# Kernel optimization log

Measured on AMD Instinct MI355X. Metric: run time of the kernel, lower is better.

## Reference

```python
import jax, jax.numpy as jnp
import numpy as np

N = 8192
F_IN = 256
F_OUT = 64
ALPHA = 0.2  # LeakyReLU negative slope
MASK_VAL = -9e15


def setup_inputs() -> dict:
    key = jax.random.key(0)
    k1, k2, k3, k4 = jax.random.split(key, 4)
    h = jax.random.normal(k1, (N, F_IN), dtype=jnp.float32)
    adj = jax.random.randint(k2, (N, N), 0, 2, dtype=jnp.int32)  # 0/1 dense adjacency
    # Parameters (original creates them inside forward with xavier init; here fixed inputs)
    W = jax.random.normal(k3, (F_IN, F_OUT), dtype=jnp.float32) * (1.414 * np.sqrt(2.0 / (F_IN + F_OUT)))
    a = jax.random.normal(k4, (2 * F_OUT, 1), dtype=jnp.float32) * (1.414 * np.sqrt(2.0 / (2 * F_OUT + 1)))
    return {"h": h, "adj": adj, "W": W, "a": a}


def reference(h, adj, W, a):
    # Wh: [N, F_OUT]
    Wh = h @ W
    # e_ij = LeakyReLU(a^T [Wh_i ; Wh_j]) computed via broadcast instead of the
    f_src = Wh @ a[:F_OUT, 0]   # [N] contribution of row node i
    f_dst = Wh @ a[F_OUT:, 0]   # [N] contribution of col node j
    e = jax.nn.leaky_relu(f_src[:, None] + f_dst[None, :], negative_slope=ALPHA)  # [N, N]
    # adj-masked row softmax
    scores = jnp.where(adj > 0, e, MASK_VAL)
    attention = jax.nn.softmax(scores, axis=1)
    # dropout omitted (deterministic eval reference)
    h_prime = attention @ Wh  # [N, F_OUT]
    return jax.nn.elu(h_prime)  # concat=True branch
```

## Files before the change

kernel.cpp:

```cpp
#include <hip/hip_runtime.h>
#include <hip/hip_bf16.h>

#define NN 8192
#define FIN 256
#define FOUT 64
#define L2E 1.4426950408889634f
#define PADK 40

typedef __attribute__((ext_vector_type(8))) short short8;
typedef __attribute__((ext_vector_type(4))) float f32x4;
typedef __attribute__((ext_vector_type(4))) int   iv4;

#define BAR() do { \
  __asm__ __volatile__("s_waitcnt lgkmcnt(0)" ::: "memory"); \
  __builtin_amdgcn_s_barrier(); \
  __asm__ __volatile__("" ::: "memory"); \
} while (0)

__device__ __forceinline__ unsigned short f2bf(float x){
  unsigned u = __float_as_uint(x);
  u += 0x7FFFu + ((u >> 16) & 1u);
  return (unsigned short)(u >> 16);
}

__global__ __launch_bounds__(256) void k_prep(const float* __restrict__ h,
    const float* __restrict__ W, const float* __restrict__ a,
    unsigned short* __restrict__ WhT, float* __restrict__ fs,
    float* __restrict__ fd, unsigned* __restrict__ gmax_u){
  __shared__ float Ws[128*64];
  __shared__ float hs[8][128];
  const int t = threadIdx.x, l = t & 63, wv = t >> 6;
  const int rb = blockIdx.x * 8;
  float acc0 = 0.f, acc1 = 0.f;
  for (int half = 0; half < 2; ++half){
    if (half) __syncthreads();
    for (int i = t; i < 2048; i += 256)
      ((float4*)Ws)[i] = ((const float4*)W)[half*2048 + i];
    {
      int rr = t >> 5, cc = t & 31;
      ((float4*)&hs[rr][0])[cc] =
          *(const float4*)(h + (size_t)(rb+rr)*FIN + half*128 + cc*4);
    }
    __syncthreads();
    #pragma unroll 8
    for (int k = 0; k < 128; ++k){
      float wval = Ws[k*64 + l];
      acc0 = fmaf(hs[wv*2+0][k], wval, acc0);
      acc1 = fmaf(hs[wv*2+1][k], wval, acc1);
    }
  }
  const int r0 = rb + wv*2, r1 = r0 + 1;
  float a1 = a[l], a2 = a[64 + l];
  float p0 = acc0*a1, q0 = acc0*a2, p1 = acc1*a1, q1 = acc1*a2;
  #pragma unroll
  for (int m = 1; m < 64; m <<= 1){
    p0 += __shfl_xor(p0, m); q0 += __shfl_xor(q0, m);
    p1 += __shfl_xor(p1, m); q1 += __shfl_xor(q1, m);
  }
  if (l == 0){
    fs[r0] = p0*L2E; fs[r1] = p1*L2E; fd[r0] = q0*L2E; fd[r1] = q1*L2E;
    atomicMax(gmax_u, __float_as_uint(q0*L2E + 64.0f));
    atomicMax(gmax_u, __float_as_uint(q1*L2E + 64.0f));
  }
  WhT[(size_t)l*NN + r0] = f2bf(acc0);
  WhT[(size_t)l*NN + r1] = f2bf(acc1);
}

struct ABuf { iv4 a0, a1; };

__device__ __forceinline__ void load_adj(ABuf& b, const int* __restrict__ adj,
                                         unsigned a_off, int s){
  const iv4* p = (const iv4*)(adj + a_off + s*32);
  b.a0 = __builtin_nontemporal_load(p);
  b.a1 = __builtin_nontemporal_load(p + 1);
}

__device__ __forceinline__ void attn_math(const ABuf& ab, f32x4 fv0, f32x4 fv1,
    short8 w0, short8 w1, short8 w2, short8 w3,
    float fsrL, float mL, f32x4* acc, float& s0, float& s1){
  const int   av[8] = {ab.a0.x,ab.a0.y,ab.a0.z,ab.a0.w, ab.a1.x,ab.a1.y,ab.a1.z,ab.a1.w};
  const float fv[8] = {fv0[0],fv0[1],fv0[2],fv0[3], fv1[0],fv1[1],fv1[2],fv1[3]};
  float w[8];
  #pragma unroll
  for (int j = 0; j < 8; ++j){
    float x  = fsrL + fv[j];
    float tt = fmaxf(x, 0.2f*x);
    float e  = __builtin_amdgcn_exp2f(tt - mL);
    w[j] = (av[j] != 0) ? e : 0.0f;
  }
  s0 += (w[0]+w[2]) + (w[4]+w[6]);
  s1 += (w[1]+w[3]) + (w[5]+w[7]);
  short8 af;
  __hip_bfloat162* afp = (__hip_bfloat162*)&af;
  #pragma unroll
  for (int j = 0; j < 4; ++j)
    afp[j] = __float22bfloat162_rn(make_float2(w[2*j], w[2*j+1]));
  acc[0] = __builtin_amdgcn_mfma_f32_16x16x32_bf16(af, w0, acc[0], 0,0,0);
  acc[1] = __builtin_amdgcn_mfma_f32_16x16x32_bf16(af, w1, acc[1], 0,0,0);
  acc[2] = __builtin_amdgcn_mfma_f32_16x16x32_bf16(af, w2, acc[2], 0,0,0);
  acc[3] = __builtin_amdgcn_mfma_f32_16x16x32_bf16(af, w3, acc[3], 0,0,0);
}

__global__ __launch_bounds__(256, 4) void k_attn(const int* __restrict__ adj,
    const unsigned short* __restrict__ WhT, const float* __restrict__ fs,
    const float* __restrict__ fd, const unsigned* __restrict__ gmax_u,
    float* __restrict__ acc_out, float* __restrict__ s_out){
  __shared__ unsigned short bslab[2][64*PADK];
  __shared__ float fslab[2][32];
  const int t = threadIdx.x, l = t & 63, wv = t >> 6;
  const int g = blockIdx.x & 127;
  const int kchunk = blockIdx.x >> 7;
  const int row = l & 15, quad = l >> 4;
  const int ibase = g*64 + wv*16;
  const int irow  = ibase + row;
  const float gmaxL = __uint_as_float(*gmax_u) - 64.0f;
  const float fsrL  = fs[irow];
  const float xL    = fsrL + gmaxL;
  const float mL    = fmaxf(xL, 0.2f*xL);

  const unsigned jbase = (unsigned)kchunk*1024u;
  const unsigned a_off = (unsigned)irow*8192u + jbase + (unsigned)quad*8u;
  const unsigned sg_off = (unsigned)l*8192u + jbase + (unsigned)wv*8u;
  const int      sl_off = l*PADK + wv*8;

  f32x4 acc[4];
  #pragma unroll
  for (int nb = 0; nb < 4; ++nb) acc[nb] = (f32x4){0.f,0.f,0.f,0.f};

  {
    short8 v = *(const short8*)(WhT + sg_off);
    *(short8*)&bslab[0][sl_off] = v;
    if (t < 32) fslab[0][t] = fd[jbase + t];
  }
  ABuf ab0, ab1;
  load_adj(ab0, adj, a_off, 0);
  load_adj(ab1, adj, a_off, 1);

  float s0 = 0.f, s1 = 0.f;
  short8 nw; float nf = 0.f;

  #pragma unroll 1
  for (int s = 0; s < 32; s += 2){
    BAR();
    nw = *(const short8*)(WhT + sg_off + (s+1)*32);
    if (t < 32) nf = fd[jbase + (s+1)*32 + t];
    {
      f32x4 fv0 = *(const f32x4*)&fslab[0][quad*8];
      f32x4 fv1 = *(const f32x4*)&fslab[0][quad*8 + 4];
      short8 w0 = *(const short8*)&bslab[0][( 0 + row)*PADK + quad*8];
      short8 w1 = *(const short8*)&bslab[0][(16 + row)*PADK + quad*8];
      short8 w2 = *(const short8*)&bslab[0][(32 + row)*PADK + quad*8];
      short8 w3 = *(const short8*)&bslab[0][(48 + row)*PADK + quad*8];
      attn_math(ab0, fv0, fv1, w0, w1, w2, w3, fsrL, mL, acc, s0, s1);
    }
    if (s + 2 < 32) load_adj(ab0, adj, a_off, s + 2);
    *(short8*)&bslab[1][sl_off] = nw;
    if (t < 32) fslab[1][t] = nf;

    BAR();
    if (s + 2 < 32){
      nw = *(const short8*)(WhT + sg_off + (s+2)*32);
      if (t < 32) nf = fd[jbase + (s+2)*32 + t];
    }
    {
      f32x4 fv0 = *(const f32x4*)&fslab[1][quad*8];
      f32x4 fv1 = *(const f32x4*)&fslab[1][quad*8 + 4];
      short8 w0 = *(const short8*)&bslab[1][( 0 + row)*PADK + quad*8];
      short8 w1 = *(const short8*)&bslab[1][(16 + row)*PADK + quad*8];
      short8 w2 = *(const short8*)&bslab[1][(32 + row)*PADK + quad*8];
      short8 w3 = *(const short8*)&bslab[1][(48 + row)*PADK + quad*8];
      attn_math(ab1, fv0, fv1, w0, w1, w2, w3, fsrL, mL, acc, s0, s1);
    }
    if (s + 3 < 32) load_adj(ab1, adj, a_off, s + 3);
    if (s + 2 < 32){
      *(short8*)&bslab[0][sl_off] = nw;
      if (t < 32) fslab[0][t] = nf;
    }
  }

  float sacc = s0 + s1;
  sacc += __shfl_xor(sacc, 16);
  sacc += __shfl_xor(sacc, 32);
  if (l < 16) s_out[kchunk*NN + ibase + l] = sacc;
  float* op = acc_out + ((size_t)kchunk*NN + ibase)*FOUT;
  #pragma unroll
  for (int nb = 0; nb < 4; ++nb)
    #pragma unroll
    for (int r = 0; r < 4; ++r)
      op[(quad*4 + r)*FOUT + nb*16 + row] = acc[nb][r];
}

__global__ __launch_bounds__(256) void k_out(const float* __restrict__ acc,
    const float* __restrict__ s, float* __restrict__ out){
  const int idx = blockIdx.x*256 + threadIdx.x;
  const int i = idx >> 6;
  float num = 0.f, den = 0.f;
  #pragma unroll
  for (int ks = 0; ks < 8; ++ks){
    num += acc[idx + (size_t)ks*(NN*FOUT)];
    den += s[i + ks*NN];
  }
  float x = num / den;
  out[idx] = (x > 0.f) ? x : (__expf(x) - 1.0f);
}

extern "C" void kernel_launch(void* const* d_in, const int* in_sizes, int n_in,
                              void* d_out, int out_size, void* d_ws, size_t ws_size,
                              hipStream_t stream){
  const float* h   = (const float*)d_in[0];
  const int*   adj = (const int*)d_in[1];
  const float* W   = (const float*)d_in[2];
  const float* a   = (const float*)d_in[3];
  char* ws = (char*)d_ws;
  unsigned short* WhT = (unsigned short*)ws;
  float*    fs     = (float*)(ws + (1u<<20));
  float*    fd     = (float*)(ws + (1u<<20) + 32768);
  unsigned* gmax_u = (unsigned*)(ws + (1u<<20) + 65536);
  float*    acc    = (float*)(ws + (2u<<20));
  float*    s_ws   = (float*)(ws + (20u<<20));

  (void)hipMemsetAsync(gmax_u, 0, 4, stream);
  k_prep<<<1024, 256, 0, stream>>>(h, W, a, WhT, fs, fd, gmax_u);
  k_attn<<<1024, 256, 0, stream>>>(adj, WhT, fs, fd, gmax_u, acc, s_ws);
  k_out<<<2048, 256, 0, stream>>>(acc, s_ws, (float*)d_out);
}
```

Measured before the change: 497.1 us.

## Pack adjacency into a bitmask in prep kernel and read bits in attention

The prep kernel gains 2048 extra blocks that read the int32 adjacency matrix once and pack it into a 1-bit-per-entry mask in workspace. The attention kernel then reads 32-bit mask words instead of 32 bytes of int32 adjacency per eight columns, so its inner loop is no longer limited by adjacency bandwidth. The full 256 MB adjacency is still read once, but now in a separate streaming pass that adds an 8 MB mask write and a kernel-boundary dependency. Total memory traffic stays about the same; the gain depends on whether the attention loop was bandwidth-bound or latency-bound on adjacency loads.

```diff
diff --git a/kernel.cpp b/kernel.cpp
--- a/kernel.cpp
+++ b/kernel.cpp
@@ -23,62 +23,74 @@
   return (unsigned short)(u >> 16);
 }
 
-__global__ __launch_bounds__(256) void k_prep(const float* __restrict__ h,
+__global__ __launch_bounds__(256) void k_pm(const float* __restrict__ h,
     const float* __restrict__ W, const float* __restrict__ a,
-    unsigned short* __restrict__ WhT, float* __restrict__ fs,
-    float* __restrict__ fd, unsigned* __restrict__ gmax_u){
+    const int* __restrict__ adj, unsigned short* __restrict__ WhT,
+    float* __restrict__ fs, float* __restrict__ fd,
+    unsigned* __restrict__ gmax_u, unsigned* __restrict__ mask){
   __shared__ float Ws[128*64];
   __shared__ float hs[8][128];
-  const int t = threadIdx.x, l = t & 63, wv = t >> 6;
-  const int rb = blockIdx.x * 8;
-  float acc0 = 0.f, acc1 = 0.f;
-  for (int half = 0; half < 2; ++half){
-    if (half) __syncthreads();
-    for (int i = t; i < 2048; i += 256)
-      ((float4*)Ws)[i] = ((const float4*)W)[half*2048 + i];
-    {
-      int rr = t >> 5, cc = t & 31;
-      ((float4*)&hs[rr][0])[cc] =
-          *(const float4*)(h + (size_t)(rb+rr)*FIN + half*128 + cc*4);
-    }
-    __syncthreads();
-    #pragma unroll 8
-    for (int k = 0; k < 128; ++k){
-      float wval = Ws[k*64 + l];
-      acc0 = fmaf(hs[wv*2+0][k], wval, acc0);
-      acc1 = fmaf(hs[wv*2+1][k], wval, acc1);
-    }
-  }
-  const int r0 = rb + wv*2, r1 = r0 + 1;
-  float a1 = a[l], a2 = a[64 + l];
-  float p0 = acc0*a1, q0 = acc0*a2, p1 = acc1*a1, q1 = acc1*a2;
-  #pragma unroll
-  for (int m = 1; m < 64; m <<= 1){
-    p0 += __shfl_xor(p0, m); q0 += __shfl_xor(q0, m);
-    p1 += __shfl_xor(p1, m); q1 += __shfl_xor(q1, m);
-  }
-  if (l == 0){
-    fs[r0] = p0*L2E; fs[r1] = p1*L2E; fd[r0] = q0*L2E; fd[r1] = q1*L2E;
-    atomicMax(gmax_u, __float_as_uint(q0*L2E + 64.0f));
-    atomicMax(gmax_u, __float_as_uint(q1*L2E + 64.0f));
-  }
-  WhT[(size_t)l*NN + r0] = f2bf(acc0);
-  WhT[(size_t)l*NN + r1] = f2bf(acc1);
-}
-
-struct ABuf { iv4 a0, a1; };
-
-__device__ __forceinline__ void load_adj(ABuf& b, const int* __restrict__ adj,
-                                         unsigned a_off, int s){
-  const iv4* p = (const iv4*)(adj + a_off + s*32);
-  b.a0 = __builtin_nontemporal_load(p);
-  b.a1 = __builtin_nontemporal_load(p + 1);
-}
-
-__device__ __forceinline__ void attn_math(const ABuf& ab, f32x4 fv0, f32x4 fv1,
+  const int bid = blockIdx.x, t = threadIdx.x;
+  if (bid < 1024){
+    const int l = t & 63, wv = t >> 6;
+    const int rb = bid * 8;
+    float acc0 = 0.f, acc1 = 0.f;
+    for (int half = 0; half < 2; ++half){
+      if (half) __syncthreads();
+      for (int i = t; i < 2048; i += 256)
+        ((float4*)Ws)[i] = ((const float4*)W)[half*2048 + i];
+      {
+        int rr = t >> 5, cc = t & 31;
+        ((float4*)&hs[rr][0])[cc] =
+            *(const float4*)(h + (size_t)(rb+rr)*FIN + half*128 + cc*4);
+      }
+      __syncthreads();
+      #pragma unroll 8
+      for (int k = 0; k < 128; ++k){
+        float wval = Ws[k*64 + l];
+        acc0 = fmaf(hs[wv*2+0][k], wval, acc0);
+        acc1 = fmaf(hs[wv*2+1][k], wval, acc1);
+      }
+    }
+    const int r0 = rb + wv*2, r1 = r0 + 1;
+    float a1 = a[l], a2 = a[64 + l];
+    float p0 = acc0*a1, q0 = acc0*a2, p1 = acc1*a1, q1 = acc1*a2;
+    #pragma unroll
+    for (int m = 1; m < 64; m <<= 1){
+      p0 += __shfl_xor(p0, m); q0 += __shfl_xor(q0, m);
+      p1 += __shfl_xor(p1, m); q1 += __shfl_xor(q1, m);
+    }
+    if (l == 0){
+      fs[r0] = p0*L2E; fs[r1] = p1*L2E; fd[r0] = q0*L2E; fd[r1] = q1*L2E;
+      atomicMax(gmax_u, __float_as_uint(q0*L2E + 64.0f));
+      atomicMax(gmax_u, __float_as_uint(q1*L2E + 64.0f));
+    }
+    WhT[(size_t)l*NN + r0] = f2bf(acc0);
+    WhT[(size_t)l*NN + r1] = f2bf(acc1);
+  } else {
+    unsigned char* nib = (unsigned char*)Ws;
+    const unsigned b2 = (unsigned)(bid - 1024);
+    #pragma unroll 1
+    for (int it = 0; it < 16; ++it){
+      const unsigned jb = (b2*16u + (unsigned)it) * 2048u;
+      const iv4* p = (const iv4*)(adj + jb + (unsigned)t*8u);
+      iv4 A = __builtin_nontemporal_load(p);
+      iv4 B = __builtin_nontemporal_load(p + 1);
+      unsigned by = (unsigned)(A.x!=0)        | ((unsigned)(A.y!=0)<<1)
+                  | ((unsigned)(A.z!=0)<<2)   | ((unsigned)(A.w!=0)<<3)
+                  | ((unsigned)(B.x!=0)<<4)   | ((unsigned)(B.y!=0)<<5)
+                  | ((unsigned)(B.z!=0)<<6)   | ((unsigned)(B.w!=0)<<7);
+      if (it) __syncthreads();
+      nib[t] = (unsigned char)by;
+      __syncthreads();
+      if (t < 64) mask[(jb >> 5) + t] = ((const unsigned*)nib)[t];
+    }
+  }
+}
+
+__device__ __forceinline__ void attn_math(unsigned mbits, f32x4 fv0, f32x4 fv1,
     short8 w0, short8 w1, short8 w2, short8 w3,
     float fsrL, float mL, f32x4* acc, float& s0, float& s1){
-  const int   av[8] = {ab.a0.x,ab.a0.y,ab.a0.z,ab.a0.w, ab.a1.x,ab.a1.y,ab.a1.z,ab.a1.w};
   const float fv[8] = {fv0[0],fv0[1],fv0[2],fv0[3], fv1[0],fv1[1],fv1[2],fv1[3]};
   float w[8];
   #pragma unroll
@@ -86,7 +98,7 @@
     float x  = fsrL + fv[j];
     float tt = fmaxf(x, 0.2f*x);
     float e  = __builtin_amdgcn_exp2f(tt - mL);
-    w[j] = (av[j] != 0) ? e : 0.0f;
+    w[j] = (mbits & (1u << j)) ? e : 0.0f;
   }
   s0 += (w[0]+w[2]) + (w[4]+w[6]);
   s1 += (w[1]+w[3]) + (w[5]+w[7]);
@@ -101,7 +113,7 @@
   acc[3] = __builtin_amdgcn_mfma_f32_16x16x32_bf16(af, w3, acc[3], 0,0,0);
 }
 
-__global__ __launch_bounds__(256, 4) void k_attn(const int* __restrict__ adj,
+__global__ __launch_bounds__(256, 4) void k_attn(const unsigned* __restrict__ mask,
     const unsigned short* __restrict__ WhT, const float* __restrict__ fs,
     const float* __restrict__ fd, const unsigned* __restrict__ gmax_u,
     float* __restrict__ acc_out, float* __restrict__ s_out){
@@ -119,9 +131,10 @@
   const float mL    = fmaxf(xL, 0.2f*xL);
 
   const unsigned jbase = (unsigned)kchunk*1024u;
-  const unsigned a_off = (unsigned)irow*8192u + jbase + (unsigned)quad*8u;
+  const unsigned m_off = (unsigned)irow*256u + (jbase >> 5);
   const unsigned sg_off = (unsigned)l*8192u + jbase + (unsigned)wv*8u;
   const int      sl_off = l*PADK + wv*8;
+  const int      qsh    = quad*8;
 
   f32x4 acc[4];
   #pragma unroll
@@ -132,9 +145,8 @@
     *(short8*)&bslab[0][sl_off] = v;
     if (t < 32) fslab[0][t] = fd[jbase + t];
   }
-  ABuf ab0, ab1;
-  load_adj(ab0, adj, a_off, 0);
-  load_adj(ab1, adj, a_off, 1);
+  unsigned m0 = mask[m_off + 0] >> qsh;
+  unsigned m1 = mask[m_off + 1] >> qsh;
 
   float s0 = 0.f, s1 = 0.f;
   short8 nw; float nf = 0.f;
@@ -145,15 +157,15 @@
     nw = *(const short8*)(WhT + sg_off + (s+1)*32);
     if (t < 32) nf = fd[jbase + (s+1)*32 + t];
     {
-      f32x4 fv0 = *(const f32x4*)&fslab[0][quad*8];
-      f32x4 fv1 = *(const f32x4*)&fslab[0][quad*8 + 4];
-      short8 w0 = *(const short8*)&bslab[0][( 0 + row)*PADK + quad*8];
-      short8 w1 = *(const short8*)&bslab[0][(16 + row)*PADK + quad*8];
-      short8 w2 = *(const short8*)&bslab[0][(32 + row)*PADK + quad*8];
-      short8 w3 = *(const short8*)&bslab[0][(48 + row)*PADK + quad*8];
-      attn_math(ab0, fv0, fv1, w0, w1, w2, w3, fsrL, mL, acc, s0, s1);
-    }
-    if (s + 2 < 32) load_adj(ab0, adj, a_off, s + 2);
+      f32x4 fv0 = *(const f32x4*)&fslab[0][qsh];
+      f32x4 fv1 = *(const f32x4*)&fslab[0][qsh + 4];
+      short8 w0 = *(const short8*)&bslab[0][( 0 + row)*PADK + qsh];
+      short8 w1 = *(const short8*)&bslab[0][(16 + row)*PADK + qsh];
+      short8 w2 = *(const short8*)&bslab[0][(32 + row)*PADK + qsh];
+      short8 w3 = *(const short8*)&bslab[0][(48 + row)*PADK + qsh];
+      attn_math(m0, fv0, fv1, w0, w1, w2, w3, fsrL, mL, acc, s0, s1);
+    }
+    if (s + 2 < 32) m0 = mask[m_off + s + 2] >> qsh;
     *(short8*)&bslab[1][sl_off] = nw;
     if (t < 32) fslab[1][t] = nf;
 
@@ -163,15 +175,15 @@
       if (t < 32) nf = fd[jbase + (s+2)*32 + t];
     }
     {
-      f32x4 fv0 = *(const f32x4*)&fslab[1][quad*8];
-      f32x4 fv1 = *(const f32x4*)&fslab[1][quad*8 + 4];
-      short8 w0 = *(const short8*)&bslab[1][( 0 + row)*PADK + quad*8];
-      short8 w1 = *(const short8*)&bslab[1][(16 + row)*PADK + quad*8];
-      short8 w2 = *(const short8*)&bslab[1][(32 + row)*PADK + quad*8];
-      short8 w3 = *(const short8*)&bslab[1][(48 + row)*PADK + quad*8];
-      attn_math(ab1, fv0, fv1, w0, w1, w2, w3, fsrL, mL, acc, s0, s1);
-    }
-    if (s + 3 < 32) load_adj(ab1, adj, a_off, s + 3);
+      f32x4 fv0 = *(const f32x4*)&fslab[1][qsh];
+      f32x4 fv1 = *(const f32x4*)&fslab[1][qsh + 4];
+      short8 w0 = *(const short8*)&bslab[1][( 0 + row)*PADK + qsh];
+      short8 w1 = *(const short8*)&bslab[1][(16 + row)*PADK + qsh];
+      short8 w2 = *(const short8*)&bslab[1][(32 + row)*PADK + qsh];
+      short8 w3 = *(const short8*)&bslab[1][(48 + row)*PADK + qsh];
+      attn_math(m1, fv0, fv1, w0, w1, w2, w3, fsrL, mL, acc, s0, s1);
+    }
+    if (s + 3 < 32) m1 = mask[m_off + s + 3] >> qsh;
     if (s + 2 < 32){
       *(short8*)&bslab[0][sl_off] = nw;
       if (t < 32) fslab[0][t] = nf;
@@ -218,9 +230,10 @@
   unsigned* gmax_u = (unsigned*)(ws + (1u<<20) + 65536);
   float*    acc    = (float*)(ws + (2u<<20));
   float*    s_ws   = (float*)(ws + (20u<<20));
+  unsigned* mask   = (unsigned*)(ws + (48u<<20));
 
   (void)hipMemsetAsync(gmax_u, 0, 4, stream);
-  k_prep<<<1024, 256, 0, stream>>>(h, W, a, WhT, fs, fd, gmax_u);
-  k_attn<<<1024, 256, 0, stream>>>(adj, WhT, fs, fd, gmax_u, acc, s_ws);
+  k_pm<<<3072, 256, 0, stream>>>(h, W, a, adj, WhT, fs, fd, gmax_u, mask);
+  k_attn<<<1024, 256, 0, stream>>>(mask, WhT, fs, fd, gmax_u, acc, s_ws);
   k_out<<<2048, 256, 0, stream>>>(acc, s_ws, (float*)d_out);
 }
```

Result: no change. 491.5 us (-1.1%).
